# Performance work log

Measured on AMD Instinct MI355X. Metric: run time of the kernel, lower is better.

The kernel has to match this reference:

```python
import jax, jax.numpy as jnp
import numpy as np

B, N, C, H = 2, 2048, 768, 12
HD = C // H
SCALE = HD ** -0.5


def setup_inputs() -> dict:
    key = jax.random.key(0)
    k1, k2, k3, k4 = jax.random.split(key, 4)
    return {
        "x": jax.random.normal(k1, (B, N, C), dtype=jnp.float32),
        "qkv_w": jax.random.normal(k2, (3 * C, C), dtype=jnp.float32) * (C ** -0.5),
        "proj_w": jax.random.normal(k3, (C, C), dtype=jnp.float32) * (C ** -0.5),
        "proj_b": jax.random.normal(k4, (C,), dtype=jnp.float32) * 0.01,
    }


def reference(x, qkv_w, proj_w, proj_b):
    b, n, c = x.shape
    # qkv: Linear(dim, 3*dim, bias=False) -> (B,N,3,H,HD) -> per-tensor (B,H,N,HD)
    qkv = (x @ qkv_w.T).reshape(b, n, 3, H, HD)
    q, k, v = jnp.moveaxis(qkv, 2, 0)          # each (B,N,H,HD)
    q = q.transpose(0, 2, 1, 3)                # (B,H,N,HD)
    k = k.transpose(0, 2, 1, 3)
    v = v.transpose(0, 2, 1, 3)
    attn_logits = jnp.einsum("bhqd,bhkd->bhqk", q, k) * SCALE  # (B,H,N,N)
    attn = jax.nn.softmax(attn_logits, axis=-1)
    score = jnp.mean(attn, axis=1)             # (B,N,N) mean over heads
    # dropout p=0.0 -> identity
    out = jnp.einsum("bhqk,bhkd->bhqd", attn, v)  # (B,H,N,HD)
    out = out.transpose(0, 2, 1, 3).reshape(b, n, c)
    out = out @ proj_w.T + proj_b
    return out, score
```

## Files before the change

### kernel.cpp

```cpp
#include <hip/hip_runtime.h>
#include <cstddef>

typedef __attribute__((ext_vector_type(8))) short bf16x8;
typedef __attribute__((ext_vector_type(4))) float f32x4;

constexpr int Bb = 2, Nn = 2048, Cc = 768, Hh = 12, HDd = 64;
constexpr float QSCALE = 0.125f * 1.44269504088896340736f;

#define VMCNT(n) asm volatile("s_waitcnt vmcnt(" #n ")" ::: "memory")
#define SBAR() __builtin_amdgcn_s_barrier()

__device__ inline short f2bf(float f) {
  unsigned u = __builtin_bit_cast(unsigned, f);
  u += 0x7fff + ((u >> 16) & 1);
  return (short)(u >> 16);
}
__device__ inline unsigned cvtpk(float a, float b) {
  unsigned r;
  asm("v_cvt_pk_bf16_f32 %0, %1, %2" : "=v"(r) : "v"(a), "v"(b));
  return r;
}
__device__ inline void gl_lds16(const void* g, void* l) {
  __builtin_amdgcn_global_load_lds(
      (const __attribute__((address_space(1))) unsigned*)g,
      (__attribute__((address_space(3))) unsigned*)l, 16, 0, 0);
}
__device__ inline bf16x8 lds8(const short* p) { return *(const bf16x8*)p; }
__device__ inline bf16x8 ld_frag(const short* base, int row, int ch) {
  return *(const bf16x8*)&base[row * 64 + (((ch ^ (row & 7)) << 3))];
}

__global__ __launch_bounds__(256) void cvt_kernel(const float* __restrict__ s,
                                                  short* __restrict__ d) {
  const int i = (blockIdx.x * 256 + threadIdx.x) * 4;
  const float4 v = *(const float4*)&s[i];
  short4 o;
  o.x = f2bf(v.x); o.y = f2bf(v.y); o.z = f2bf(v.z); o.w = f2bf(v.w);
  *(short4*)&d[i] = o;
}

__global__ __launch_bounds__(256) void qkv_mfma(
    const short* __restrict__ A, const short* __restrict__ W,
    short* __restrict__ Qg, short* __restrict__ Kg, short* __restrict__ Vtg) {
  __shared__ short As[2 * 8192];
  __shared__ short Bs[2 * 8192];
  const int t = threadIdx.x, l = t & 63, w = t >> 6;
  const int lr = l & 15, lh = l >> 4;
  const int m0 = blockIdx.x * 128, r0 = blockIdx.y * 128;
  const int wr = w >> 1, wc = w & 1;
  f32x4 acc[4][4];
#pragma unroll
  for (int i = 0; i < 4; ++i)
#pragma unroll
    for (int j = 0; j < 4; ++j) acc[i][j] = (f32x4){0.f, 0.f, 0.f, 0.f};

  auto stage = [&](const int buf, const int kt) {
#pragma unroll
    for (int u = 0; u < 4; ++u) {
      const int du = (w * 4 + u) * 64 + l;
      const int row = du >> 3, ch = du & 7, sch = ch ^ (row & 7);
      gl_lds16(A + (size_t)(m0 + row) * Cc + kt * 64 + sch * 8,
               &As[buf * 8192 + (w * 4 + u) * 512]);
      gl_lds16(W + (size_t)(r0 + row) * Cc + kt * 64 + sch * 8,
               &Bs[buf * 8192 + (w * 4 + u) * 512]);
    }
  };
  auto compute = [&](const int buf) {
    const short* Ab = As + buf * 8192;
    const short* Bbp = Bs + buf * 8192;
#pragma unroll
    for (int kp = 0; kp < 2; ++kp) {
      bf16x8 af[4], bfv[4];
#pragma unroll
      for (int i = 0; i < 4; ++i)
        af[i] = ld_frag(Ab, wr * 64 + i * 16 + lr, kp * 4 + lh);
#pragma unroll
      for (int j = 0; j < 4; ++j)
        bfv[j] = ld_frag(Bbp, wc * 64 + j * 16 + lr, kp * 4 + lh);
      __builtin_amdgcn_s_setprio(1);
#pragma unroll
      for (int i = 0; i < 4; ++i)
#pragma unroll
        for (int j = 0; j < 4; ++j)
          acc[i][j] = __builtin_amdgcn_mfma_f32_16x16x32_bf16(
              af[i], bfv[j], acc[i][j], 0, 0, 0);
      __builtin_amdgcn_s_setprio(0);
    }
  };

  stage(0, 0);
#pragma unroll 1
  for (int kk = 0; kk < 10; kk += 2) {
    stage(1, kk + 1);
    VMCNT(8); SBAR();
    compute(0);
    SBAR();
    stage(0, kk + 2);
    VMCNT(8); SBAR();
    compute(1);
    SBAR();
  }
  stage(1, 11);
  VMCNT(8); SBAR();
  compute(0);
  SBAR();
  VMCNT(0); SBAR();
  compute(1);

  const int which = r0 / Cc;
  const int rbase = r0 % Cc;
  const int bq = m0 >> 11;
  const int nb = (m0 & 2047) + wr * 64;
  if (which == 2) {
#pragma unroll
    for (int j = 0; j < 4; ++j) {
      const int rr = rbase + wc * 64 + j * 16 + lr;
      const int head = rr >> 6, dd = rr & 63;
      short* vp = &Vtg[(((size_t)bq * Hh + head) * HDd + dd) * Nn];
#pragma unroll
      for (int i = 0; i < 4; ++i) {
        short4 o;
        o.x = f2bf(acc[i][j][0]); o.y = f2bf(acc[i][j][1]);
        o.z = f2bf(acc[i][j][2]); o.w = f2bf(acc[i][j][3]);
        *(short4*)&vp[nb + i * 16 + lh * 4] = o;
      }
    }
  } else {
    const float scl = (which == 0) ? QSCALE : 1.0f;
    short* __restrict__ dst = (which == 0) ? Qg : Kg;
#pragma unroll
    for (int j = 0; j < 4; ++j) {
      const int rr = rbase + wc * 64 + j * 16 + lr;
      const int head = rr >> 6, dd = rr & 63;
      short* dp = &dst[((size_t)bq * Hh + head) * Nn * HDd + dd];
#pragma unroll
      for (int i = 0; i < 4; ++i)
#pragma unroll
        for (int r = 0; r < 4; ++r)
          dp[(size_t)(nb + i * 16 + lh * 4 + r) * HDd] =
              f2bf(acc[i][j][r] * scl);
    }
  }
}

__global__ __launch_bounds__(256, 3) void attn_pass1(
    const short* __restrict__ Qg, const short* __restrict__ Kg,
    const short* __restrict__ Vtg, float* __restrict__ Linv,
    short* __restrict__ OHb) {
  __shared__ short SM[4 * 4096 + 4 * 1024];
  const int t = threadIdx.x, l = t & 63, w = t >> 6;
  const int lr = l & 15, lh = l >> 4;
  const int raw = blockIdx.x;
  const int bid = (raw & 7) * 96 + (raw >> 3);
  const int q0 = (bid & 31) * 64;
  const int head = (bid >> 5) % Hh;
  const int b = bid / (32 * Hh);
  const size_t base = (size_t)b * Hh + head;
  const short* Qh = Qg + base * Nn * HDd;
  const short* Kh = Kg + base * Nn * HDd;
  const short* Vh = Vtg + base * HDd * Nn;
  const int qw = q0 + w * 16;
  const int PB = 16384 + w * 1024;

  const bf16x8 onesf = {0x3F80, 0x3F80, 0x3F80, 0x3F80,
                        0x3F80, 0x3F80, 0x3F80, 0x3F80};

  int fof[2][4], wofi[4], pof[2];
#pragma unroll
  for (int kp = 0; kp < 2; ++kp) {
#pragma unroll
    for (int i = 0; i < 4; ++i)
      fof[kp][i] = (i * 16 + lr) * 64 + (((kp * 4 + lh) ^ (lr & 7)) << 3);
    pof[kp] = lr * 64 + (((kp * 4 + lh) ^ (lr & 7)) << 3);
  }
#pragma unroll
  for (int i = 0; i < 4; ++i) {
    const int ch = 2 * i + (lh >> 1);
    wofi[i] = lr * 64 + ((ch ^ (lr & 7)) << 3) + (lh & 1) * 4;
  }

  bf16x8 qf[2];
#pragma unroll
  for (int kp = 0; kp < 2; ++kp)
    qf[kp] = *(const bf16x8*)&Qh[(size_t)(qw + lr) * HDd + kp * 32 + lh * 8];

  f32x4 accO[4], accL;
  accL = (f32x4){0.f, 0.f, 0.f, 0.f};
#pragma unroll
  for (int j = 0; j < 4; ++j) accO[j] = (f32x4){0.f, 0.f, 0.f, 0.f};

  auto stage = [&](const int buf, const int tile) {
    const short* Kt = Kh + (size_t)tile * (64 * HDd);
    const short* Vt = Vh + tile * 64;
#pragma unroll
    for (int u = 0; u < 2; ++u) {
      const int cu = u * 4 + w;
      const int du = cu * 64 + l;
      const int row = du >> 3, ch = du & 7, sch = ch ^ (row & 7);
      gl_lds16(Kt + row * 64 + sch * 8, &SM[buf * 4096 + cu * 512]);
      gl_lds16(Vt + (size_t)row * Nn + sch * 8,
               &SM[8192 + buf * 4096 + cu * 512]);
    }
  };

  auto compute = [&](const int kb) {
    const int vb = 8192 + kb;
    f32x4 sacc[4];
#pragma unroll
    for (int i = 0; i < 4; ++i) sacc[i] = (f32x4){0.f, 0.f, 0.f, 0.f};
    __builtin_amdgcn_s_setprio(1);
#pragma unroll
    for (int kp = 0; kp < 2; ++kp)
#pragma unroll
      for (int i = 0; i < 4; ++i)
        sacc[i] = __builtin_amdgcn_mfma_f32_16x16x32_bf16(
            lds8(&SM[kb + fof[kp][i]]), qf[kp], sacc[i], 0, 0, 0);
    __builtin_amdgcn_s_setprio(0);
#pragma unroll
    for (int i = 0; i < 4; ++i) {
      const float p0 = exp2f(sacc[i][0]), p1 = exp2f(sacc[i][1]);
      const float p2 = exp2f(sacc[i][2]), p3 = exp2f(sacc[i][3]);
      uint2 pk;
      pk.x = cvtpk(p0, p1);
      pk.y = cvtpk(p2, p3);
      *(uint2*)&SM[PB + wofi[i]] = pk;
    }
    __builtin_amdgcn_s_setprio(1);
#pragma unroll
    for (int kp = 0; kp < 2; ++kp) {
      const bf16x8 pa = lds8(&SM[PB + pof[kp]]);
      accL = __builtin_amdgcn_mfma_f32_16x16x32_bf16(pa, onesf, accL, 0, 0, 0);
#pragma unroll
      for (int j = 0; j < 4; ++j)
        accO[j] = __builtin_amdgcn_mfma_f32_16x16x32_bf16(
            pa, lds8(&SM[vb + fof[kp][j]]), accO[j], 0, 0, 0);
    }
    __builtin_amdgcn_s_setprio(0);
  };

  stage(0, 0);
#pragma unroll 1
  for (int it = 0; it < 30; it += 2) {
    stage(1, it + 1);
    VMCNT(4); SBAR();
    compute(0);
    SBAR();
    stage(0, it + 2);
    VMCNT(4); SBAR();
    compute(4096);
    SBAR();
  }
  stage(1, 31);
  VMCNT(4); SBAR();
  compute(0);
  SBAR();
  VMCNT(0); SBAR();
  compute(4096);

  f32x4 linvq;
#pragma unroll
  for (int r = 0; r < 4; ++r) linvq[r] = 1.0f / accL[r];
  if (lr == 0) *(f32x4*)&Linv[base * Nn + qw + 4 * lh] = linvq;
#pragma unroll
  for (int j = 0; j < 4; ++j)
#pragma unroll
    for (int r = 0; r < 4; ++r)
      OHb[((size_t)b * Nn + qw + 4 * lh + r) * Cc + head * HDd + j * 16 + lr] =
          f2bf(accO[j][r] * linvq[r]);
}

__global__ __launch_bounds__(256, 4) void score_mfma(
    const short* __restrict__ Qg, const short* __restrict__ Kg,
    const float* __restrict__ Linv, float* __restrict__ score) {
  __shared__ __align__(16) char SMraw[64 * 68 * 4];
  short* SK = (short*)SMraw;
  float* SMf = (float*)SMraw;
  const int t = threadIdx.x, l = t & 63, w = t >> 6;
  const int lr = l & 15, lh = l >> 4;
  const int raw = blockIdx.x;
  const int xcd = raw & 7, idx = raw >> 3;
  const int b = xcd >> 2;
  const int q0 = ((xcd & 3) * 8 + (idx >> 5)) * 64;
  const int kv0 = (idx & 31) * 64;
  const int qw = q0 + w * 16;

  int fof[2][4];
#pragma unroll
  for (int kp = 0; kp < 2; ++kp)
#pragma unroll
    for (int i = 0; i < 4; ++i)
      fof[kp][i] = (i * 16 + lr) * 64 + (((kp * 4 + lh) ^ (lr & 7)) << 3);

  f32x4 sc[4];
#pragma unroll
  for (int i = 0; i < 4; ++i) sc[i] = (f32x4){0.f, 0.f, 0.f, 0.f};

  auto stage = [&](const int kb, const int h) {
    const short* Kt = Kg + (((size_t)b * Hh + h) * Nn + kv0) * HDd;
#pragma unroll
    for (int u = 0; u < 2; ++u) {
      const int cu = u * 4 + w;
      const int du = cu * 64 + l;
      const int row = du >> 3, ch = du & 7, sch = ch ^ (row & 7);
      gl_lds16(Kt + row * 64 + sch * 8, &SK[kb + cu * 512]);
    }
  };
  auto ldqQ = [&](const int h, bf16x8& a0, bf16x8& a1) {
    const size_t hb = (size_t)b * Hh + h;
    a0 = *(const bf16x8*)&Qg[(hb * Nn + qw + lr) * HDd + lh * 8];
    a1 = *(const bf16x8*)&Qg[(hb * Nn + qw + lr) * HDd + 32 + lh * 8];
  };
  auto qk = [&](const int kb, const bf16x8 a0, const bf16x8 a1,
                f32x4 (&sacc)[4]) {
#pragma unroll
    for (int i = 0; i < 4; ++i) sacc[i] = (f32x4){0.f, 0.f, 0.f, 0.f};
#pragma unroll
    for (int i = 0; i < 4; ++i)
      sacc[i] = __builtin_amdgcn_mfma_f32_16x16x32_bf16(
          lds8(&SK[kb + fof[0][i]]), a0, sacc[i], 0, 0, 0);
#pragma unroll
    for (int i = 0; i < 4; ++i)
      sacc[i] = __builtin_amdgcn_mfma_f32_16x16x32_bf16(
          lds8(&SK[kb + fof[1][i]]), a1, sacc[i], 0, 0, 0);
  };
  auto expacc = [&](const f32x4 (&sacc)[4], const float lv) {
#pragma unroll
    for (int i = 0; i < 4; ++i)
#pragma unroll
      for (int r = 0; r < 4; ++r) sc[i][r] += exp2f(sacc[i][r]) * lv;
  };

  bf16x8 qA0, qA1, qB0, qB1;
  float lvA, lvB;
  f32x4 sA[4], sB[4];
  stage(0, 0);
  ldqQ(0, qA0, qA1);
  __syncthreads();
  stage(4096, 1);
  ldqQ(1, qB0, qB1);
  lvA = Linv[((size_t)b * Hh + 0) * Nn + qw + lr];
  qk(0, qA0, qA1, sA);
  __syncthreads();
#pragma unroll 1
  for (int h = 1; h < 11; h += 2) {
    stage(0, h + 1);
    ldqQ(h + 1, qA0, qA1);
    lvB = Linv[((size_t)b * Hh + h) * Nn + qw + lr];
    qk(4096, qB0, qB1, sB);
    expacc(sA, lvA);
    __syncthreads();
    stage(4096, h + 2);
    ldqQ(h + 2, qB0, qB1);
    lvA = Linv[((size_t)b * Hh + h + 1) * Nn + qw + lr];
    qk(0, qA0, qA1, sA);
    expacc(sB, lvB);
    __syncthreads();
  }
  lvB = Linv[((size_t)b * Hh + 11) * Nn + qw + lr];
  qk(4096, qB0, qB1, sB);
  expacc(sA, lvA);
  expacc(sB, lvB);
  __syncthreads();

  constexpr float invH = 1.0f / 12.0f;
#pragma unroll
  for (int i = 0; i < 4; ++i) {
    f32x4 o;
#pragma unroll
    for (int r = 0; r < 4; ++r) o[r] = sc[i][r] * invH;
    *(f32x4*)&SMf[(w * 16 + lr) * 68 + i * 16 + 4 * lh] = o;
  }
  __syncthreads();
#pragma unroll
  for (int s = 0; s < 4; ++s) {
    const int lin = t + s * 256;
    const int row = lin >> 4, ch = lin & 15;
    const f32x4 v = *(const f32x4*)&SMf[row * 68 + ch * 4];
    *(f32x4*)&score[((size_t)b * Nn + q0 + row) * Nn + kv0 + ch * 4] = v;
  }
}

__global__ __launch_bounds__(256) void proj_mfma(
    const short* __restrict__ A, const short* __restrict__ W,
    const float* __restrict__ bias, float* __restrict__ out) {
  __shared__ short As[128 * 64];
  __shared__ short Bs[128 * 64];
  const int t = threadIdx.x, l = t & 63, w = t >> 6;
  const int lr = l & 15, lh = l >> 4;
  const int m0 = blockIdx.x * 128, c0 = blockIdx.y * 128;
  const int wr = w >> 1, wc = w & 1;
  f32x4 acc[4][4];
#pragma unroll
  for (int i = 0; i < 4; ++i)
#pragma unroll
    for (int j = 0; j < 4; ++j) acc[i][j] = (f32x4){0.f, 0.f, 0.f, 0.f};

  for (int k0 = 0; k0 < Cc; k0 += 64) {
    __syncthreads();
#pragma unroll
    for (int u = 0; u < 4; ++u) {
      const int du = (w * 4 + u) * 64 + l;
      const int row = du >> 3, ch = du & 7, sch = ch ^ (row & 7);
      gl_lds16(A + (size_t)(m0 + row) * Cc + k0 + sch * 8,
               &As[(w * 4 + u) * 512]);
      gl_lds16(W + (size_t)(c0 + row) * Cc + k0 + sch * 8,
               &Bs[(w * 4 + u) * 512]);
    }
    __syncthreads();
#pragma unroll
    for (int kp = 0; kp < 2; ++kp) {
      bf16x8 af[4], bfv[4];
#pragma unroll
      for (int i = 0; i < 4; ++i)
        af[i] = ld_frag(As, wr * 64 + i * 16 + lr, kp * 4 + lh);
#pragma unroll
      for (int j = 0; j < 4; ++j)
        bfv[j] = ld_frag(Bs, wc * 64 + j * 16 + lr, kp * 4 + lh);
#pragma unroll
      for (int i = 0; i < 4; ++i)
#pragma unroll
        for (int j = 0; j < 4; ++j)
          acc[i][j] = __builtin_amdgcn_mfma_f32_16x16x32_bf16(
              af[i], bfv[j], acc[i][j], 0, 0, 0);
    }
  }
#pragma unroll
  for (int j = 0; j < 4; ++j) {
    const int c = c0 + wc * 64 + j * 16 + lr;
    const float bi = bias[c];
#pragma unroll
    for (int i = 0; i < 4; ++i)
#pragma unroll
      for (int r = 0; r < 4; ++r) {
        const int m = m0 + wr * 64 + i * 16 + lh * 4 + r;
        out[(size_t)m * Cc + c] = acc[i][j][r] + bi;
      }
  }
}

extern "C" void kernel_launch(void* const* d_in, const int* in_sizes, int n_in,
                              void* d_out, int out_size, void* d_ws,
                              size_t ws_size, hipStream_t stream) {
  const float* x = (const float*)d_in[0];
  const float* qkv_w = (const float*)d_in[1];
  const float* proj_w = (const float*)d_in[2];
  const float* proj_b = (const float*)d_in[3];

  float* out = (float*)d_out;
  float* score = out + (size_t)Bb * Nn * Cc;

  const size_t nx = (size_t)Bb * Nn * Cc;
  const size_t nwq = (size_t)3 * Cc * Cc;
  const size_t npw = (size_t)Cc * Cc;
  short* xb = (short*)d_ws;
  short* wqb = xb + nx;
  short* pwb = wqb + nwq;
  short* Qb = pwb + npw;
  short* Kb = Qb + nx;
  short* Vtb = Kb + nx;
  short* OHb = Vtb + nx;
  float* Linv = (float*)(OHb + nx);

  cvt_kernel<<<dim3((int)(nx / 1024)), 256, 0, stream>>>(x, xb);
  cvt_kernel<<<dim3((int)(nwq / 1024)), 256, 0, stream>>>(qkv_w, wqb);
  cvt_kernel<<<dim3((int)(npw / 1024)), 256, 0, stream>>>(proj_w, pwb);
  qkv_mfma<<<dim3(32, 18), 256, 0, stream>>>(xb, wqb, Qb, Kb, Vtb);
  attn_pass1<<<dim3(768), 256, 0, stream>>>(Qb, Kb, Vtb, Linv, OHb);
  score_mfma<<<dim3(2048), 256, 0, stream>>>(Qb, Kb, Linv, score);
  proj_mfma<<<dim3(32, 6), 256, 0, stream>>>(OHb, pwb, proj_b, out);
}
```

Baseline: 141.2 us.

## Split attention KV range across two blocks with 32x32 MFMA and combine pass

```diff
diff --git a/kernel.cpp b/kernel.cpp
--- a/kernel.cpp
+++ b/kernel.cpp
@@ -2,9 +2,14 @@
 #include <cstddef>
 
 typedef __attribute__((ext_vector_type(8))) short bf16x8;
+typedef __attribute__((ext_vector_type(8))) short short8v;
 typedef __attribute__((ext_vector_type(4))) float f32x4;
+typedef __attribute__((ext_vector_type(16))) float f32x16;
+typedef __attribute__((ext_vector_type(4))) unsigned u32x4;
 
 constexpr int Bb = 2, Nn = 2048, Cc = 768, Hh = 12, HDd = 64;
+constexpr int BHN = Bb * Hh * Nn;
+constexpr size_t BNC = (size_t)Bb * Nn * Cc;
 constexpr float QSCALE = 0.125f * 1.44269504088896340736f;
 
 #define VMCNT(n) asm volatile("s_waitcnt vmcnt(" #n ")" ::: "memory")
@@ -15,17 +20,34 @@
   u += 0x7fff + ((u >> 16) & 1);
   return (short)(u >> 16);
 }
+__device__ inline float bf2f(short s) {
+  unsigned u = ((unsigned)(unsigned short)s) << 16;
+  return __builtin_bit_cast(float, u);
+}
 __device__ inline unsigned cvtpk(float a, float b) {
   unsigned r;
   asm("v_cvt_pk_bf16_f32 %0, %1, %2" : "=v"(r) : "v"(a), "v"(b));
   return r;
 }
+__device__ inline void pl32swap(unsigned& a, unsigned& b) {
+  asm("v_permlane32_swap_b32 %0, %1" : "+v"(a), "+v"(b));
+}
 __device__ inline void gl_lds16(const void* g, void* l) {
   __builtin_amdgcn_global_load_lds(
       (const __attribute__((address_space(1))) unsigned*)g,
       (__attribute__((address_space(3))) unsigned*)l, 16, 0, 0);
 }
 __device__ inline bf16x8 lds8(const short* p) { return *(const bf16x8*)p; }
+__device__ inline bf16x8 mk8(unsigned a, unsigned b, unsigned c, unsigned d) {
+  u32x4 t = {a, b, c, d};
+  return __builtin_bit_cast(bf16x8, t);
+}
+__device__ inline f32x16 zero16() {
+  f32x16 z;
+#pragma unroll
+  for (int r = 0; r < 16; ++r) z[r] = 0.f;
+  return z;
+}
 __device__ inline bf16x8 ld_frag(const short* base, int row, int ch) {
   return *(const bf16x8*)&base[row * 64 + (((ch ^ (row & 7)) << 3))];
 }
@@ -143,55 +165,44 @@
   }
 }
 
-__global__ __launch_bounds__(256, 3) void attn_pass1(
+__global__ __launch_bounds__(256, 3) void attn_pass1_split(
     const short* __restrict__ Qg, const short* __restrict__ Kg,
-    const short* __restrict__ Vtg, float* __restrict__ Linv,
-    short* __restrict__ OHb) {
-  __shared__ short SM[4 * 4096 + 4 * 1024];
+    const short* __restrict__ Vtg, float* __restrict__ Lpart,
+    short* __restrict__ OHp) {
+  __shared__ short SM[4 * 4096];
   const int t = threadIdx.x, l = t & 63, w = t >> 6;
-  const int lr = l & 15, lh = l >> 4;
+  const int lo5 = l & 31, hi5 = l >> 5;
   const int raw = blockIdx.x;
   const int bid = (raw & 7) * 96 + (raw >> 3);
-  const int q0 = (bid & 31) * 64;
+  const int split = bid & 1;
+  const int qt = (bid >> 1) & 15;
   const int head = (bid >> 5) % Hh;
-  const int b = bid / (32 * Hh);
+  const int b = (bid >> 5) / Hh;
   const size_t base = (size_t)b * Hh + head;
   const short* Qh = Qg + base * Nn * HDd;
   const short* Kh = Kg + base * Nn * HDd;
   const short* Vh = Vtg + base * HDd * Nn;
-  const int qw = q0 + w * 16;
-  const int PB = 16384 + w * 1024;
-
-  const bf16x8 onesf = {0x3F80, 0x3F80, 0x3F80, 0x3F80,
-                        0x3F80, 0x3F80, 0x3F80, 0x3F80};
-
-  int fof[2][4], wofi[4], pof[2];
-#pragma unroll
-  for (int kp = 0; kp < 2; ++kp) {
-#pragma unroll
-    for (int i = 0; i < 4; ++i)
-      fof[kp][i] = (i * 16 + lr) * 64 + (((kp * 4 + lh) ^ (lr & 7)) << 3);
-    pof[kp] = lr * 64 + (((kp * 4 + lh) ^ (lr & 7)) << 3);
-  }
-#pragma unroll
-  for (int i = 0; i < 4; ++i) {
-    const int ch = 2 * i + (lh >> 1);
-    wofi[i] = lr * 64 + ((ch ^ (lr & 7)) << 3) + (lh & 1) * 4;
-  }
-
-  bf16x8 qf[2];
-#pragma unroll
-  for (int kp = 0; kp < 2; ++kp)
-    qf[kp] = *(const bf16x8*)&Qh[(size_t)(qw + lr) * HDd + kp * 32 + lh * 8];
-
-  f32x4 accO[4], accL;
-  accL = (f32x4){0.f, 0.f, 0.f, 0.f};
-#pragma unroll
-  for (int j = 0; j < 4; ++j) accO[j] = (f32x4){0.f, 0.f, 0.f, 0.f};
+  const int qw = qt * 128 + w * 32;
+  const int kvbase = split * 1024;
+
+  int of2[2][4];
+#pragma unroll
+  for (int i = 0; i < 2; ++i)
+#pragma unroll
+    for (int s = 0; s < 4; ++s)
+      of2[i][s] = (i * 32 + lo5) * 64 + ((((2 * s + hi5) ^ (l & 7))) << 3);
+
+  bf16x8 qf[4];
+#pragma unroll
+  for (int s = 0; s < 4; ++s)
+    qf[s] = *(const bf16x8*)&Qh[(size_t)(qw + lo5) * HDd + s * 16 + hi5 * 8];
+
+  f32x16 accO0 = zero16(), accO1 = zero16();
+  float Lp = 0.f;
 
   auto stage = [&](const int buf, const int tile) {
-    const short* Kt = Kh + (size_t)tile * (64 * HDd);
-    const short* Vt = Vh + tile * 64;
+    const short* Kt = Kh + (size_t)(kvbase + tile * 64) * HDd;
+    const short* Vt = Vh + kvbase + tile * 64;
 #pragma unroll
     for (int u = 0; u < 2; ++u) {
       const int cu = u * 4 + w;
@@ -205,42 +216,61 @@
 
   auto compute = [&](const int kb) {
     const int vb = 8192 + kb;
-    f32x4 sacc[4];
-#pragma unroll
-    for (int i = 0; i < 4; ++i) sacc[i] = (f32x4){0.f, 0.f, 0.f, 0.f};
+    f32x16 s0 = zero16(), s1 = zero16();
     __builtin_amdgcn_s_setprio(1);
 #pragma unroll
-    for (int kp = 0; kp < 2; ++kp)
-#pragma unroll
-      for (int i = 0; i < 4; ++i)
-        sacc[i] = __builtin_amdgcn_mfma_f32_16x16x32_bf16(
-            lds8(&SM[kb + fof[kp][i]]), qf[kp], sacc[i], 0, 0, 0);
+    for (int s = 0; s < 4; ++s)
+      s0 = __builtin_amdgcn_mfma_f32_32x32x16_bf16(lds8(&SM[kb + of2[0][s]]),
+                                                   qf[s], s0, 0, 0, 0);
+#pragma unroll
+    for (int s = 0; s < 4; ++s)
+      s1 = __builtin_amdgcn_mfma_f32_32x32x16_bf16(lds8(&SM[kb + of2[1][s]]),
+                                                   qf[s], s1, 0, 0, 0);
     __builtin_amdgcn_s_setprio(0);
-#pragma unroll
-    for (int i = 0; i < 4; ++i) {
-      const float p0 = exp2f(sacc[i][0]), p1 = exp2f(sacc[i][1]);
-      const float p2 = exp2f(sacc[i][2]), p3 = exp2f(sacc[i][3]);
-      uint2 pk;
-      pk.x = cvtpk(p0, p1);
-      pk.y = cvtpk(p2, p3);
-      *(uint2*)&SM[PB + wofi[i]] = pk;
-    }
+    float p[16];
+#pragma unroll
+    for (int r = 0; r < 16; ++r) { p[r] = exp2f(s0[r]); Lp += p[r]; }
+    unsigned a0 = cvtpk(p[0], p[1]), b0 = cvtpk(p[2], p[3]);
+    unsigned c0 = cvtpk(p[4], p[5]), d0 = cvtpk(p[6], p[7]);
+    pl32swap(a0, c0); pl32swap(b0, d0);
+    const bf16x8 pa0 = mk8(a0, b0, c0, d0);
+    unsigned a1 = cvtpk(p[8], p[9]), b1 = cvtpk(p[10], p[11]);
+    unsigned c1 = cvtpk(p[12], p[13]), d1 = cvtpk(p[14], p[15]);
+    pl32swap(a1, c1); pl32swap(b1, d1);
+    const bf16x8 pa1 = mk8(a1, b1, c1, d1);
+#pragma unroll
+    for (int r = 0; r < 16; ++r) { p[r] = exp2f(s1[r]); Lp += p[r]; }
+    unsigned a2 = cvtpk(p[0], p[1]), b2 = cvtpk(p[2], p[3]);
+    unsigned c2 = cvtpk(p[4], p[5]), d2 = cvtpk(p[6], p[7]);
+    pl32swap(a2, c2); pl32swap(b2, d2);
+    const bf16x8 pa2 = mk8(a2, b2, c2, d2);
+    unsigned a3 = cvtpk(p[8], p[9]), b3 = cvtpk(p[10], p[11]);
+    unsigned c3 = cvtpk(p[12], p[13]), d3 = cvtpk(p[14], p[15]);
+    pl32swap(a3, c3); pl32swap(b3, d3);
+    const bf16x8 pa3 = mk8(a3, b3, c3, d3);
     __builtin_amdgcn_s_setprio(1);
-#pragma unroll
-    for (int kp = 0; kp < 2; ++kp) {
-      const bf16x8 pa = lds8(&SM[PB + pof[kp]]);
-      accL = __builtin_amdgcn_mfma_f32_16x16x32_bf16(pa, onesf, accL, 0, 0, 0);
-#pragma unroll
-      for (int j = 0; j < 4; ++j)
-        accO[j] = __builtin_amdgcn_mfma_f32_16x16x32_bf16(
-            pa, lds8(&SM[vb + fof[kp][j]]), accO[j], 0, 0, 0);
-    }
+    accO0 = __builtin_amdgcn_mfma_f32_32x32x16_bf16(lds8(&SM[vb + of2[0][0]]),
+                                                    pa0, accO0, 0, 0, 0);
+    accO1 = __builtin_amdgcn_mfma_f32_32x32x16_bf16(lds8(&SM[vb + of2[1][0]]),
+                                                    pa0, accO1, 0, 0, 0);
+    accO0 = __builtin_amdgcn_mfma_f32_32x32x16_bf16(lds8(&SM[vb + of2[0][1]]),
+                                                    pa1, accO0, 0, 0, 0);
+    accO1 = __builtin_amdgcn_mfma_f32_32x32x16_bf16(lds8(&SM[vb + of2[1][1]]),
+                                                    pa1, accO1, 0, 0, 0);
+    accO0 = __builtin_amdgcn_mfma_f32_32x32x16_bf16(lds8(&SM[vb + of2[0][2]]),
+                                                    pa2, accO0, 0, 0, 0);
+    accO1 = __builtin_amdgcn_mfma_f32_32x32x16_bf16(lds8(&SM[vb + of2[1][2]]),
+                                                    pa2, accO1, 0, 0, 0);
+    accO0 = __builtin_amdgcn_mfma_f32_32x32x16_bf16(lds8(&SM[vb + of2[0][3]]),
+                                                    pa3, accO0, 0, 0, 0);
+    accO1 = __builtin_amdgcn_mfma_f32_32x32x16_bf16(lds8(&SM[vb + of2[1][3]]),
+                                                    pa3, accO1, 0, 0, 0);
     __builtin_amdgcn_s_setprio(0);
   };
 
   stage(0, 0);
 #pragma unroll 1
-  for (int it = 0; it < 30; it += 2) {
+  for (int it = 0; it < 14; it += 2) {
     stage(1, it + 1);
     VMCNT(4); SBAR();
     compute(0);
@@ -250,23 +280,55 @@
     compute(4096);
     SBAR();
   }
-  stage(1, 31);
+  stage(1, 15);
   VMCNT(4); SBAR();
   compute(0);
   SBAR();
   VMCNT(0); SBAR();
   compute(4096);
 
-  f32x4 linvq;
-#pragma unroll
-  for (int r = 0; r < 4; ++r) linvq[r] = 1.0f / accL[r];
-  if (lr == 0) *(f32x4*)&Linv[base * Nn + qw + 4 * lh] = linvq;
-#pragma unroll
-  for (int j = 0; j < 4; ++j)
-#pragma unroll
-    for (int r = 0; r < 4; ++r)
-      OHb[((size_t)b * Nn + qw + 4 * lh + r) * Cc + head * HDd + j * 16 + lr] =
-          f2bf(accO[j][r] * linvq[r]);
+  Lp += __shfl_xor(Lp, 32);
+  const int qv = qw + lo5;
+  if (hi5 == 0) Lpart[(size_t)split * BHN + base * Nn + qv] = Lp;
+  short* OHs = OHp + (size_t)split * BNC;
+#pragma unroll
+  for (int dh = 0; dh < 2; ++dh) {
+#pragma unroll
+    for (int g = 0; g < 4; ++g) {
+      short4 o;
+      if (dh == 0) {
+        o.x = f2bf(accO0[4 * g + 0]); o.y = f2bf(accO0[4 * g + 1]);
+        o.z = f2bf(accO0[4 * g + 2]); o.w = f2bf(accO0[4 * g + 3]);
+      } else {
+        o.x = f2bf(accO1[4 * g + 0]); o.y = f2bf(accO1[4 * g + 1]);
+        o.z = f2bf(accO1[4 * g + 2]); o.w = f2bf(accO1[4 * g + 3]);
+      }
+      *(short4*)&OHs[((size_t)b * Nn + qv) * Cc + head * HDd + dh * 32 +
+                     8 * g + 4 * hi5] = o;
+    }
+  }
+}
+
+__global__ __launch_bounds__(256) void combine_kernel(
+    short* __restrict__ OHp, const float* __restrict__ Lpart,
+    float* __restrict__ Linv) {
+  const int tid = blockIdx.x * 256 + threadIdx.x;
+  const int c8 = tid % 96;
+  const int c = c8 * 8;
+  const int mn = tid / 96;
+  const int n = mn & 2047, b = mn >> 11;
+  const int head = c >> 6;
+  const int li = ((b * Hh + head) << 11) + n;
+  const float lsum = Lpart[li] + Lpart[BHN + li];
+  const float inv = 1.0f / lsum;
+  const size_t off = (size_t)mn * Cc + c;
+  const short8v o0 = *(const short8v*)&OHp[off];
+  const short8v o1 = *(const short8v*)&OHp[BNC + off];
+  short8v o;
+#pragma unroll
+  for (int e = 0; e < 8; ++e) o[e] = f2bf((bf2f(o0[e]) + bf2f(o1[e])) * inv);
+  *(short8v*)&OHp[off] = o;
+  if ((c & 63) == 0) Linv[li] = inv;
 }
 
 __global__ __launch_bounds__(256, 4) void score_mfma(
@@ -447,9 +509,9 @@
   const float* proj_b = (const float*)d_in[3];
 
   float* out = (float*)d_out;
-  float* score = out + (size_t)Bb * Nn * Cc;
-
-  const size_t nx = (size_t)Bb * Nn * Cc;
+  float* score = out + BNC;
+
+  const size_t nx = BNC;
   const size_t nwq = (size_t)3 * Cc * Cc;
   const size_t npw = (size_t)Cc * Cc;
   short* xb = (short*)d_ws;
@@ -458,14 +520,17 @@
   short* Qb = pwb + npw;
   short* Kb = Qb + nx;
   short* Vtb = Kb + nx;
-  short* OHb = Vtb + nx;
-  float* Linv = (float*)(OHb + nx);
+  short* OHp = Vtb + nx;
+  float* Lpart = (float*)(OHp + 2 * nx);
+  float* Linv = Lpart + 2 * BHN;
 
   cvt_kernel<<<dim3((int)(nx / 1024)), 256, 0, stream>>>(x, xb);
   cvt_kernel<<<dim3((int)(nwq / 1024)), 256, 0, stream>>>(qkv_w, wqb);
   cvt_kernel<<<dim3((int)(npw / 1024)), 256, 0, stream>>>(proj_w, pwb);
   qkv_mfma<<<dim3(32, 18), 256, 0, stream>>>(xb, wqb, Qb, Kb, Vtb);
-  attn_pass1<<<dim3(768), 256, 0, stream>>>(Qb, Kb, Vtb, Linv, OHb);
+  attn_pass1_split<<<dim3(768), 256, 0, stream>>>(Qb, Kb, Vtb, Lpart, OHp);
+  combine_kernel<<<dim3((int)(nx / 8 / 256)), 256, 0, stream>>>(OHp, Lpart,
+                                                                Linv);
   score_mfma<<<dim3(2048), 256, 0, stream>>>(Qb, Kb, Linv, score);
-  proj_mfma<<<dim3(32, 6), 256, 0, stream>>>(OHb, pwb, proj_b, out);
-}
+  proj_mfma<<<dim3(32, 6), 256, 0, stream>>>(OHp, pwb, proj_b, out);
+}
```

Result: slower. 144.3 us (+2.2%).

## Enlarge score kernel tile to 256 queries per block for K reuse

Applied to the files above, without the earlier changes.

```diff
diff --git a/kernel.cpp b/kernel.cpp
--- a/kernel.cpp
+++ b/kernel.cpp
@@ -269,20 +269,21 @@
           f2bf(accO[j][r] * linvq[r]);
 }
 
-__global__ __launch_bounds__(256, 4) void score_mfma(
+__global__ __launch_bounds__(256, 2) void score_mfma(
     const short* __restrict__ Qg, const short* __restrict__ Kg,
     const float* __restrict__ Linv, float* __restrict__ score) {
-  __shared__ __align__(16) char SMraw[64 * 68 * 4];
+  __shared__ __align__(16) char SMraw[256 * 36 * 4];
   short* SK = (short*)SMraw;
-  float* SMf = (float*)SMraw;
+  float* SOUT = (float*)SMraw;
   const int t = threadIdx.x, l = t & 63, w = t >> 6;
   const int lr = l & 15, lh = l >> 4;
   const int raw = blockIdx.x;
-  const int xcd = raw & 7, idx = raw >> 3;
-  const int b = xcd >> 2;
-  const int q0 = ((xcd & 3) * 8 + (idx >> 5)) * 64;
-  const int kv0 = (idx & 31) * 64;
-  const int qw = q0 + w * 16;
+  const int bid = (raw & 7) * 64 + (raw >> 3);
+  const int b = bid >> 8;
+  const int qt = (bid >> 5) & 7;
+  const int kv0 = (bid & 31) * 64;
+  const int q0 = qt * 256;
+  const int qw = q0 + w * 64;
 
   int fof[2][4];
 #pragma unroll
@@ -291,9 +292,11 @@
     for (int i = 0; i < 4; ++i)
       fof[kp][i] = (i * 16 + lr) * 64 + (((kp * 4 + lh) ^ (lr & 7)) << 3);
 
-  f32x4 sc[4];
-#pragma unroll
-  for (int i = 0; i < 4; ++i) sc[i] = (f32x4){0.f, 0.f, 0.f, 0.f};
+  f32x4 sc[4][4];
+#pragma unroll
+  for (int i = 0; i < 4; ++i)
+#pragma unroll
+    for (int j = 0; j < 4; ++j) sc[i][j] = (f32x4){0.f, 0.f, 0.f, 0.f};
 
   auto stage = [&](const int kb, const int h) {
     const short* Kt = Kg + (((size_t)b * Hh + h) * Nn + kv0) * HDd;
@@ -305,78 +308,77 @@
       gl_lds16(Kt + row * 64 + sch * 8, &SK[kb + cu * 512]);
     }
   };
-  auto ldqQ = [&](const int h, bf16x8& a0, bf16x8& a1) {
-    const size_t hb = (size_t)b * Hh + h;
-    a0 = *(const bf16x8*)&Qg[(hb * Nn + qw + lr) * HDd + lh * 8];
-    a1 = *(const bf16x8*)&Qg[(hb * Nn + qw + lr) * HDd + 32 + lh * 8];
-  };
-  auto qk = [&](const int kb, const bf16x8 a0, const bf16x8 a1,
-                f32x4 (&sacc)[4]) {
-#pragma unroll
-    for (int i = 0; i < 4; ++i) sacc[i] = (f32x4){0.f, 0.f, 0.f, 0.f};
-#pragma unroll
-    for (int i = 0; i < 4; ++i)
-      sacc[i] = __builtin_amdgcn_mfma_f32_16x16x32_bf16(
-          lds8(&SK[kb + fof[0][i]]), a0, sacc[i], 0, 0, 0);
-#pragma unroll
-    for (int i = 0; i < 4; ++i)
-      sacc[i] = __builtin_amdgcn_mfma_f32_16x16x32_bf16(
-          lds8(&SK[kb + fof[1][i]]), a1, sacc[i], 0, 0, 0);
-  };
-  auto expacc = [&](const f32x4 (&sacc)[4], const float lv) {
-#pragma unroll
-    for (int i = 0; i < 4; ++i)
-#pragma unroll
-      for (int r = 0; r < 4; ++r) sc[i][r] += exp2f(sacc[i][r]) * lv;
-  };
-
-  bf16x8 qA0, qA1, qB0, qB1;
-  float lvA, lvB;
-  f32x4 sA[4], sB[4];
+
   stage(0, 0);
-  ldqQ(0, qA0, qA1);
-  __syncthreads();
-  stage(4096, 1);
-  ldqQ(1, qB0, qB1);
-  lvA = Linv[((size_t)b * Hh + 0) * Nn + qw + lr];
-  qk(0, qA0, qA1, sA);
   __syncthreads();
 #pragma unroll 1
-  for (int h = 1; h < 11; h += 2) {
-    stage(0, h + 1);
-    ldqQ(h + 1, qA0, qA1);
-    lvB = Linv[((size_t)b * Hh + h) * Nn + qw + lr];
-    qk(4096, qB0, qB1, sB);
-    expacc(sA, lvA);
+  for (int h = 0; h < Hh; ++h) {
+    if (h + 1 < Hh) stage(((h + 1) & 1) * 4096, h + 1);
+    const size_t hb = (size_t)b * Hh + h;
+    bf16x8 qf[2][4];
+    float lv[4];
+#pragma unroll
+    for (int j = 0; j < 4; ++j) {
+      qf[0][j] =
+          *(const bf16x8*)&Qg[(hb * Nn + qw + j * 16 + lr) * HDd + lh * 8];
+      qf[1][j] = *(const bf16x8*)&Qg[(hb * Nn + qw + j * 16 + lr) * HDd + 32 +
+                                     lh * 8];
+      lv[j] = Linv[hb * Nn + qw + j * 16 + lr];
+    }
+    const int kb = (h & 1) * 4096;
+#pragma unroll
+    for (int ih = 0; ih < 4; ih += 2) {
+      f32x4 sacc[2][4];
+#pragma unroll
+      for (int ii = 0; ii < 2; ++ii)
+#pragma unroll
+        for (int j = 0; j < 4; ++j) sacc[ii][j] = (f32x4){0.f, 0.f, 0.f, 0.f};
+      __builtin_amdgcn_s_setprio(1);
+#pragma unroll
+      for (int kp = 0; kp < 2; ++kp)
+#pragma unroll
+        for (int ii = 0; ii < 2; ++ii) {
+          const bf16x8 kf = lds8(&SK[kb + fof[kp][ih + ii]]);
+#pragma unroll
+          for (int j = 0; j < 4; ++j)
+            sacc[ii][j] = __builtin_amdgcn_mfma_f32_16x16x32_bf16(
+                kf, qf[kp][j], sacc[ii][j], 0, 0, 0);
+        }
+      __builtin_amdgcn_s_setprio(0);
+#pragma unroll
+      for (int ii = 0; ii < 2; ++ii)
+#pragma unroll
+        for (int j = 0; j < 4; ++j)
+#pragma unroll
+          for (int r = 0; r < 4; ++r)
+            sc[ih + ii][j][r] += exp2f(sacc[ii][j][r]) * lv[j];
+    }
     __syncthreads();
-    stage(4096, h + 2);
-    ldqQ(h + 2, qB0, qB1);
-    lvA = Linv[((size_t)b * Hh + h + 1) * Nn + qw + lr];
-    qk(0, qA0, qA1, sA);
-    expacc(sB, lvB);
+  }
+
+  constexpr float invH = 1.0f / 12.0f;
+#pragma unroll
+  for (int h0 = 0; h0 < 2; ++h0) {
+#pragma unroll
+    for (int ii = 0; ii < 2; ++ii)
+#pragma unroll
+      for (int j = 0; j < 4; ++j) {
+        f32x4 o;
+#pragma unroll
+        for (int r = 0; r < 4; ++r) o[r] = sc[h0 * 2 + ii][j][r] * invH;
+        const int ql = w * 64 + j * 16 + lr;
+        *(f32x4*)&SOUT[ql * 36 + ii * 16 + 4 * lh] = o;
+      }
     __syncthreads();
-  }
-  lvB = Linv[((size_t)b * Hh + 11) * Nn + qw + lr];
-  qk(4096, qB0, qB1, sB);
-  expacc(sA, lvA);
-  expacc(sB, lvB);
-  __syncthreads();
-
-  constexpr float invH = 1.0f / 12.0f;
-#pragma unroll
-  for (int i = 0; i < 4; ++i) {
-    f32x4 o;
-#pragma unroll
-    for (int r = 0; r < 4; ++r) o[r] = sc[i][r] * invH;
-    *(f32x4*)&SMf[(w * 16 + lr) * 68 + i * 16 + 4 * lh] = o;
-  }
-  __syncthreads();
-#pragma unroll
-  for (int s = 0; s < 4; ++s) {
-    const int lin = t + s * 256;
-    const int row = lin >> 4, ch = lin & 15;
-    const f32x4 v = *(const f32x4*)&SMf[row * 68 + ch * 4];
-    *(f32x4*)&score[((size_t)b * Nn + q0 + row) * Nn + kv0 + ch * 4] = v;
+#pragma unroll
+    for (int s = 0; s < 8; ++s) {
+      const int unit = s * 256 + t;
+      const int row = unit >> 3, u8 = unit & 7;
+      const f32x4 v = *(const f32x4*)&SOUT[row * 36 + u8 * 4];
+      *(f32x4*)&score[((size_t)b * Nn + q0 + row) * Nn + kv0 + h0 * 32 +
+                      u8 * 4] = v;
+    }
+    __syncthreads();
   }
 }
 
@@ -466,6 +468,6 @@
   cvt_kernel<<<dim3((int)(npw / 1024)), 256, 0, stream>>>(proj_w, pwb);
   qkv_mfma<<<dim3(32, 18), 256, 0, stream>>>(xb, wqb, Qb, Kb, Vtb);
   attn_pass1<<<dim3(768), 256, 0, stream>>>(Qb, Kb, Vtb, Linv, OHb);
-  score_mfma<<<dim3(2048), 256, 0, stream>>>(Qb, Kb, Linv, score);
+  score_mfma<<<dim3(512), 256, 0, stream>>>(Qb, Kb, Linv, score);
   proj_mfma<<<dim3(32, 6), 256, 0, stream>>>(OHb, pwb, proj_b, out);
 }
```

New measurement: 148.4 us. 1.05x slower.
